# Kernel tuning notes

Hardware: AMD Instinct MI355X
Metric: run time of the kernel (lower is better)

Reference implementation:

```python
import jax, jax.numpy as jnp
import numpy as np

C = 1.0          # Poincare ball curvature
TEMP = 0.1       # softmax temperature
EPS = 1e-15
TANH_CLIP = 1.0 - 1e-5


def setup_inputs() -> dict:
    key = jax.random.key(0)
    ks = jax.random.split(key, 9)
    B, Din, H, D, P = 2048, 1024, 4096, 128, 1000
    inp = {
        "x": jax.random.normal(ks[0], (B, Din), dtype=jnp.float32),
        "W1": jax.random.normal(ks[1], (Din, H), dtype=jnp.float32) / np.sqrt(Din),
        "b1": jnp.zeros((H,), dtype=jnp.float32),
        "W2": jax.random.normal(ks[2], (H, H), dtype=jnp.float32) / np.sqrt(H),
        "b2": jnp.zeros((H,), dtype=jnp.float32),
        "W3": jax.random.normal(ks[3], (H, D), dtype=jnp.float32) / np.sqrt(H),
        "b3": jnp.zeros((D,), dtype=jnp.float32),
        # prototypes: points inside the unit ball (norm ~ 0.2)
        "prototypes": jax.random.normal(ks[4], (P, D), dtype=jnp.float32) * 0.02,
    }
    return inp


def _expmap0(u):
    sqc = np.sqrt(C)
    n = jnp.maximum(jnp.linalg.norm(u, axis=-1, keepdims=True), EPS)
    return jnp.tanh(sqc * n) * u / (sqc * n)


def _logmap0(y):
    sqc = np.sqrt(C)
    n = jnp.maximum(jnp.linalg.norm(y, axis=-1, keepdims=True), EPS)
    arg = jnp.clip(sqc * n, 0.0, TANH_CLIP)
    return jnp.arctanh(arg) * y / (sqc * n)


def _pairwise_dist(proto, xh):
    # dist(x=proto[P,D], y=xh[B,D]) = (2/sqrt(c)) * artanh(sqrt(c)*||(-x) (+) y||)
    # Mobius add norm computed from Gram products only (no [B,P,D] intermediate).
    # a = -proto, b = xh
    a2 = jnp.sum(proto * proto, axis=-1)          # [P]  ||a||^2
    b2 = jnp.sum(xh * xh, axis=-1)                # [B]  ||b||^2
    ab = -jnp.einsum('bd,pd->bp', xh, proto)      # [B,P] <a,b>
    a2_ = a2[None, :]
    b2_ = b2[:, None]
    alpha = 1.0 + 2.0 * C * ab + C * b2_
    beta = 1.0 - C * a2_
    gamma = 1.0 + 2.0 * C * ab + (C * C) * a2_ * b2_
    m2 = (alpha * alpha * a2_ + 2.0 * alpha * beta * ab + beta * beta * b2_) / (gamma * gamma)
    mnorm = jnp.sqrt(jnp.maximum(m2, 0.0))
    sqc = np.sqrt(C)
    arg = jnp.clip(sqc * mnorm, 0.0, TANH_CLIP)
    return (2.0 / sqc) * jnp.arctanh(arg)         # [B,P]


def reference(x, W1, b1, W2, b2, W3, b3, prototypes):
    h = jax.nn.gelu(x @ W1 + b1, approximate=False)
    h = jax.nn.gelu(h @ W2 + b2, approximate=False)
    u = h @ W3 + b3                               # [B,D]
    x_hyp = _expmap0(u)
    dists = _pairwise_dist(prototypes, x_hyp)     # [B,P]
    logits = -dists / TEMP
    pred = jnp.argmax(logits, axis=1)             # [B]
    pred_protos = jax.lax.stop_gradient(prototypes[pred])  # detach, as in torch
    feedback = _logmap0(pred_protos)              # [B,D]
    return logits, feedback
```

## Files before the change

kernel.cpp:

```cpp
#include <hip/hip_runtime.h>
#include <math.h>

#define B_SZ 2048
#define DIN  1024
#define H_SZ 4096
#define D_SZ 128
#define P_SZ 1000
#define PPAD 1024

typedef __attribute__((ext_vector_type(8))) short bf16x8;
typedef __attribute__((ext_vector_type(4))) float f32x4;

__device__ __forceinline__ float gelu_exact(float v) {
    return 0.5f * v * (1.0f + erff(v * 0.70710678118654752f));
}

__device__ __forceinline__ short f2bf(float f) {
    unsigned u = __float_as_uint(f);
    u = (u + 0x7fffu + ((u >> 16) & 1u)) >> 16;
    return (short)u;
}

__device__ __forceinline__ void gload_lds16(const void* g, void* l) {
    __builtin_amdgcn_global_load_lds(
        (__attribute__((address_space(1))) void*)(uintptr_t)g,
        (__attribute__((address_space(3))) void*)(uintptr_t)l,
        16, 0, 0);
}

__global__ __launch_bounds__(256) void cvt_bf16(
    const float* __restrict__ in, short* __restrict__ out, int n)
{
    const int i = (blockIdx.x * 256 + threadIdx.x) * 4;
    if (i + 3 < n) {
        const float4 v = *reinterpret_cast<const float4*>(&in[i]);
        short4 o;
        o.x = f2bf(v.x); o.y = f2bf(v.y); o.z = f2bf(v.z); o.w = f2bf(v.w);
        *reinterpret_cast<short4*>(&out[i]) = o;
    }
}

__global__ __launch_bounds__(256) void transpose_bf16(
    const float* __restrict__ W, short* __restrict__ WT, int K, int N)
{
    __shared__ float t[64][65];
    const int tid = threadIdx.x;
    const int n0 = blockIdx.x * 64, k0 = blockIdx.y * 64;

    #pragma unroll
    for (int i = 0; i < 4; ++i) {
        const int idx = i * 256 + tid;
        const int r  = idx >> 4;
        const int c4 = (idx & 15) * 4;
        const float4 v = *reinterpret_cast<const float4*>(&W[(size_t)(k0 + r) * N + n0 + c4]);
        t[r][c4 + 0] = v.x; t[r][c4 + 1] = v.y; t[r][c4 + 2] = v.z; t[r][c4 + 3] = v.w;
    }
    __syncthreads();

    #pragma unroll
    for (int i = 0; i < 2; ++i) {
        const int idx = i * 256 + tid;
        const int n  = idx >> 3;
        const int kc = (idx & 7) * 8;
        bf16x8 o;
        #pragma unroll
        for (int q = 0; q < 8; ++q) o[q] = f2bf(t[kc + q][n]);
        *reinterpret_cast<bf16x8*>(&WT[(size_t)(n0 + n) * K + k0 + kc]) = o;
    }
}

__global__ __launch_bounds__(128) void proto_prep(
    const float* __restrict__ proto, short* __restrict__ protob,
    float* __restrict__ a2gp)
{
    const int p = blockIdx.x;
    const int d = threadIdx.x;
    const float y = (p < P_SZ) ? proto[(size_t)p * D_SZ + d] : 0.f;
    protob[(size_t)p * D_SZ + d] = f2bf(y);
    float s = y * y;
    #pragma unroll
    for (int off = 32; off; off >>= 1) s += __shfl_down(s, off);
    __shared__ float part[2];
    if ((d & 63) == 0) part[d >> 6] = s;
    __syncthreads();
    if (d == 0) a2gp[p] = part[0] + part[1];
}

template<int EPI>
__global__ __launch_bounds__(512) void gemm_big(
    const short* __restrict__ A, const short* __restrict__ BT,
    const float* __restrict__ bias, void* __restrict__ Cout,
    int M, int N, int K)
{
    extern __shared__ __align__(16) char smem[];

    const int tid  = threadIdx.x;
    const int lane = tid & 63;
    const int wid  = tid >> 6;
    const int row0 = blockIdx.y * 256;
    const int col0 = blockIdx.x * 128;
    const int wm = (wid >> 1) * 64;
    const int wn = (wid & 1) * 64;
    const int lr = lane & 15, kq = lane >> 4;

    const int kpb    = K / gridDim.z;
    const int kstart = blockIdx.z * kpb;
    const int NT = kpb >> 6;

    f32x4 acc[4][4];
    #pragma unroll
    for (int i = 0; i < 4; ++i)
        #pragma unroll
        for (int j = 0; j < 4; ++j) acc[i][j] = (f32x4){0.f, 0.f, 0.f, 0.f};

    const int srow = lane >> 3;
    const int kch  = (lane & 7) ^ srow;
    const short* Ag = A  + (size_t)(row0 + wid * 32 + srow) * K + kstart + kch * 8;
    const short* Bg = BT + (size_t)(col0 + wid * 16 + srow) * K + kstart + kch * 8;

    auto stage = [&](int t) {
        const int buf = t % 3;
        char* sA = smem + buf * 49152;
        char* sB = sA + 32768;
        const int k0 = t << 6;
        #pragma unroll
        for (int ii = 0; ii < 4; ++ii)
            gload_lds16(Ag + (size_t)ii * 8 * K + k0, sA + (wid * 4 + ii) * 1024);
        #pragma unroll
        for (int ii = 0; ii < 2; ++ii)
            gload_lds16(Bg + (size_t)ii * 8 * K + k0, sB + (wid * 2 + ii) * 1024);
    };

    stage(0);
    stage(1);
    asm volatile("s_waitcnt vmcnt(6)" ::: "memory");
    __builtin_amdgcn_s_barrier();
    asm volatile("" ::: "memory");

    for (int t = 0; t < NT; ++t) {
        const bool more = (t + 2) < NT;
        if (more) stage(t + 2);

        const char* sA = smem + (t % 3) * 49152;
        const char* sB = sA + 32768;

        #pragma unroll
        for (int ks = 0; ks < 2; ++ks) {
            bf16x8 af[4], bfv[4];
            #pragma unroll
            for (int i = 0; i < 4; ++i) {
                const int row = wm + i * 16 + lr;
                af[i] = *reinterpret_cast<const bf16x8*>(
                    sA + row * 128 + (((ks * 4 + kq) ^ (lr & 7)) * 16));
            }
            #pragma unroll
            for (int j = 0; j < 4; ++j) {
                const int row = wn + j * 16 + lr;
                bfv[j] = *reinterpret_cast<const bf16x8*>(
                    sB + row * 128 + (((ks * 4 + kq) ^ (lr & 7)) * 16));
            }
            __builtin_amdgcn_s_setprio(1);
            #pragma unroll
            for (int i = 0; i < 4; ++i)
                #pragma unroll
                for (int j = 0; j < 4; ++j)
                    acc[i][j] = __builtin_amdgcn_mfma_f32_16x16x32_bf16(
                        af[i], bfv[j], acc[i][j], 0, 0, 0);
            __builtin_amdgcn_s_setprio(0);
        }

        asm volatile("" ::: "memory");
        if (more) asm volatile("s_waitcnt vmcnt(6) lgkmcnt(0)" ::: "memory");
        else      asm volatile("s_waitcnt vmcnt(0) lgkmcnt(0)" ::: "memory");
        __builtin_amdgcn_s_barrier();
        asm volatile("" ::: "memory");
    }

    #pragma unroll
    for (int j = 0; j < 4; ++j) {
        const int col = col0 + wn + j * 16 + lr;
        const float bv = (EPI == 0) ? bias[col] : 0.f;
        #pragma unroll
        for (int i = 0; i < 4; ++i) {
            #pragma unroll
            for (int q = 0; q < 4; ++q) {
                const int row = row0 + wm + i * 16 + kq * 4 + q;
                if (EPI == 0) {
                    float v = gelu_exact(acc[i][j][q] + bv);
                    ((short*)Cout)[(size_t)row * N + col] = f2bf(v);
                } else {
                    ((float*)Cout)[((size_t)blockIdx.z * M + row) * N + col] = acc[i][j][q];
                }
            }
        }
    }
}

__global__ __launch_bounds__(128) void expmap_kernel(
    const float* __restrict__ up, const float* __restrict__ b3,
    short* __restrict__ xhb, float* __restrict__ rowb2)
{
    const int b = blockIdx.x;
    const int d = threadIdx.x;
    float u = b3[d];
    #pragma unroll
    for (int z = 0; z < 16; ++z)
        u += up[((size_t)z * B_SZ + b) * D_SZ + d];

    float s = u * u;
    #pragma unroll
    for (int off = 32; off; off >>= 1) s += __shfl_down(s, off);
    __shared__ float part[2];
    if ((d & 63) == 0) part[d >> 6] = s;
    __syncthreads();
    const float n2 = part[0] + part[1];

    const float n = fmaxf(sqrtf(n2), 1e-15f);
    const float t = tanhf(n);
    xhb[(size_t)b * D_SZ + d] = f2bf(u * (t / n));
    if (d == 0) rowb2[b] = t * t;
}

__global__ __launch_bounds__(256) void dist_mfma(
    const short* __restrict__ xhb, const short* __restrict__ protob,
    const float* __restrict__ rowb2, const float* __restrict__ a2gp,
    float* __restrict__ logits)
{
    __shared__ __align__(16) char xs[128 * 256];
    __shared__ __align__(16) char ps[64 * 256];

    const int tid  = threadIdx.x;
    const int lane = tid & 63, wid = tid >> 6;
    const int pt = blockIdx.x * 64;
    const int bt = blockIdx.y * 128;
    const int wm = (wid >> 1) * 64;
    const int wn = (wid & 1) * 32;
    const int lr = lane & 15, kq = lane >> 4;

    const int rl = lane >> 4, c = lane & 15;
    #pragma unroll
    for (int i = 0; i < 8; ++i) {
        const int row = wid * 32 + i * 4 + rl;
        const int lc  = (c & 8) | ((c & 7) ^ (row & 7));
        gload_lds16(xhb + (size_t)(bt + row) * D_SZ + lc * 8,
                    xs + (wid * 8 + i) * 1024);
    }
    #pragma unroll
    for (int i = 0; i < 4; ++i) {
        const int row = wid * 16 + i * 4 + rl;
        const int lc  = (c & 8) | ((c & 7) ^ (row & 7));
        gload_lds16(protob + (size_t)(pt + row) * D_SZ + lc * 8,
                    ps + (wid * 4 + i) * 1024);
    }
    __syncthreads();

    f32x4 acc[4][2];
    #pragma unroll
    for (int i = 0; i < 4; ++i)
        #pragma unroll
        for (int j = 0; j < 2; ++j) acc[i][j] = (f32x4){0.f, 0.f, 0.f, 0.f};

    #pragma unroll
    for (int ks = 0; ks < 4; ++ks) {
        const int kslot = ks * 4 + kq;
        bf16x8 af[4], bfv[2];
        #pragma unroll
        for (int i = 0; i < 4; ++i) {
            const int row = wm + i * 16 + lr;
            const int ph = (kslot & 8) | ((kslot & 7) ^ (row & 7));
            af[i] = *reinterpret_cast<const bf16x8*>(xs + row * 256 + ph * 16);
        }
        #pragma unroll
        for (int j = 0; j < 2; ++j) {
            const int row = wn + j * 16 + lr;
            const int ph = (kslot & 8) | ((kslot & 7) ^ (row & 7));
            bfv[j] = *reinterpret_cast<const bf16x8*>(ps + row * 256 + ph * 16);
        }
        #pragma unroll
        for (int i = 0; i < 4; ++i)
            #pragma unroll
            for (int j = 0; j < 2; ++j)
                acc[i][j] = __builtin_amdgcn_mfma_f32_16x16x32_bf16(
                    af[i], bfv[j], acc[i][j], 0, 0, 0);
    }

    #pragma unroll
    for (int j = 0; j < 2; ++j) {
        const int p = pt + wn + j * 16 + lr;
        if (p < P_SZ) {
            const float a2 = a2gp[p];
            #pragma unroll
            for (int i = 0; i < 4; ++i) {
                #pragma unroll
                for (int q = 0; q < 4; ++q) {
                    const int b = bt + wm + i * 16 + kq * 4 + q;
                    const float b2 = rowb2[b];
                    const float ab = -acc[i][j][q];
                    const float alpha = 1.f + 2.f * ab + b2;
                    const float beta  = 1.f - a2;
                    const float gamma = 1.f + 2.f * ab + a2 * b2;
                    const float num = alpha * alpha * a2 + 2.f * alpha * beta * ab + beta * beta * b2;
                    const float m2 = num / (gamma * gamma);
                    const float mn = sqrtf(fmaxf(m2, 0.f));
                    const float arg = fminf(mn, 0.99999f);
                    const float dist = logf((1.f + arg) / (1.f - arg));
                    logits[(size_t)b * P_SZ + p] = -10.f * dist;
                }
            }
        }
    }
}

__global__ __launch_bounds__(256) void head_kernel(
    const float* __restrict__ logits, const float* __restrict__ proto,
    float* __restrict__ fb)
{
    const int b = blockIdx.x;
    const int tid = threadIdx.x;

    float best = -INFINITY; int bi = 0;
    for (int p = tid; p < P_SZ; p += 256) {
        const float v = logits[(size_t)b * P_SZ + p];
        if (v > best) { best = v; bi = p; }
    }
    __shared__ float bv[256];
    __shared__ int   bidx[256];
    bv[tid] = best; bidx[tid] = bi;
    __syncthreads();
    for (int s = 128; s; s >>= 1) {
        if (tid < s) {
            const float ov = bv[tid + s]; const int oi = bidx[tid + s];
            if (ov > bv[tid] || (ov == bv[tid] && oi < bidx[tid])) { bv[tid] = ov; bidx[tid] = oi; }
        }
        __syncthreads();
    }
    const int pred = bidx[0];
    __syncthreads();

    float y = 0.f;
    if (tid < 128) y = proto[(size_t)pred * D_SZ + tid];
    bv[tid] = y * y;
    __syncthreads();
    for (int s = 128; s; s >>= 1) {
        if (tid < s) bv[tid] += bv[tid + s];
        __syncthreads();
    }
    const float n2 = bv[0];
    if (tid < 128) {
        const float n = fmaxf(sqrtf(n2), 1e-15f);
        const float arg = fminf(n, 0.99999f);
        const float at = 0.5f * logf((1.f + arg) / (1.f - arg));
        fb[(size_t)b * D_SZ + tid] = at * (y / n);
    }
}

extern "C" void kernel_launch(void* const* d_in, const int* in_sizes, int n_in,
                              void* d_out, int out_size, void* d_ws, size_t ws_size,
                              hipStream_t stream)
{
    const float* x     = (const float*)d_in[0];
    const float* W1    = (const float*)d_in[1];
    const float* b1    = (const float*)d_in[2];
    const float* W2    = (const float*)d_in[3];
    const float* b2v   = (const float*)d_in[4];
    const float* W3    = (const float*)d_in[5];
    const float* b3    = (const float*)d_in[6];
    const float* proto = (const float*)d_in[7];

    float* logits = (float*)d_out;
    float* fb     = logits + (size_t)B_SZ * P_SZ;

    short* xb     = (short*)d_ws;
    short* w1t    = xb    + (size_t)B_SZ * DIN;
    short* w2t    = w1t   + (size_t)H_SZ * DIN;
    short* w3t    = w2t   + (size_t)H_SZ * H_SZ;
    short* h1     = w3t   + (size_t)D_SZ * H_SZ;
    short* h2     = h1    + (size_t)B_SZ * H_SZ;
    short* xhb    = h2    + (size_t)B_SZ * H_SZ;
    short* protob = xhb   + (size_t)B_SZ * D_SZ;
    float* rowb2  = (float*)(protob + (size_t)PPAD * D_SZ);
    float* a2gp   = rowb2 + B_SZ;
    float* up     = (float*)h1;

    static_cast<void>(hipFuncSetAttribute(
        reinterpret_cast<const void*>(&gemm_big<0>),
        hipFuncAttributeMaxDynamicSharedMemorySize, 3 * 49152));
    static_cast<void>(hipFuncSetAttribute(
        reinterpret_cast<const void*>(&gemm_big<1>),
        hipFuncAttributeMaxDynamicSharedMemorySize, 3 * 49152));

    cvt_bf16<<<(B_SZ * DIN) / 1024, 256, 0, stream>>>(x, xb, B_SZ * DIN);
    transpose_bf16<<<dim3(H_SZ / 64, DIN / 64), 256, 0, stream>>>(W1, w1t, DIN, H_SZ);
    transpose_bf16<<<dim3(H_SZ / 64, H_SZ / 64), 256, 0, stream>>>(W2, w2t, H_SZ, H_SZ);
    transpose_bf16<<<dim3(D_SZ / 64, H_SZ / 64), 256, 0, stream>>>(W3, w3t, H_SZ, D_SZ);
    proto_prep<<<PPAD, 128, 0, stream>>>(proto, protob, a2gp);

    gemm_big<0><<<dim3(H_SZ / 128, B_SZ / 256), 512, 3 * 49152, stream>>>(
        xb, w1t, b1, h1, B_SZ, H_SZ, DIN);
    gemm_big<0><<<dim3(H_SZ / 128, B_SZ / 256), 512, 3 * 49152, stream>>>(
        h1, w2t, b2v, h2, B_SZ, H_SZ, H_SZ);
    gemm_big<1><<<dim3(1, B_SZ / 256, 16), 512, 3 * 49152, stream>>>(
        h2, w3t, nullptr, up, B_SZ, D_SZ, H_SZ);

    expmap_kernel<<<B_SZ, 128, 0, stream>>>(up, b3, xhb, rowb2);
    dist_mfma<<<dim3(PPAD / 64, B_SZ / 128), 256, 0, stream>>>(
        xhb, protob, rowb2, a2gp, logits);
    head_kernel<<<B_SZ, 256, 0, stream>>>(logits, proto, fb);
}
```

Before: 272.0 us.

## Merge prep kernels into one launch and split GEMM k-step with interleaved barriers

Five preprocessing launches (x conversion, three weight transposes, prototype prep) are folded into one kernel that picks its role from the block index. This removes launch gaps and lets the small jobs run alongside the W2 transpose. Separately, the GEMM main loop now reads the first k-half's fragments before issuing the next global-to-LDS stage. It adds block barriers between the two MFMA halves, so LDS reads, global loads and MFMA can interleave across waves, at the cost of more barriers per iteration.

New measurement: 278.6 us. 2.4% more time.

```diff
diff --git a/kernel.cpp b/kernel.cpp
--- a/kernel.cpp
+++ b/kernel.cpp
@@ -28,25 +28,11 @@
         16, 0, 0);
 }
 
-__global__ __launch_bounds__(256) void cvt_bf16(
-    const float* __restrict__ in, short* __restrict__ out, int n)
-{
-    const int i = (blockIdx.x * 256 + threadIdx.x) * 4;
-    if (i + 3 < n) {
-        const float4 v = *reinterpret_cast<const float4*>(&in[i]);
-        short4 o;
-        o.x = f2bf(v.x); o.y = f2bf(v.y); o.z = f2bf(v.z); o.w = f2bf(v.w);
-        *reinterpret_cast<short4*>(&out[i]) = o;
-    }
-}
-
-__global__ __launch_bounds__(256) void transpose_bf16(
-    const float* __restrict__ W, short* __restrict__ WT, int K, int N)
-{
-    __shared__ float t[64][65];
-    const int tid = threadIdx.x;
-    const int n0 = blockIdx.x * 64, k0 = blockIdx.y * 64;
-
+__device__ __forceinline__ void trans_tile(
+    const float* __restrict__ W, short* __restrict__ WT, int K, int N,
+    int bx, int by, int tid, float (*t)[65])
+{
+    const int n0 = bx * 64, k0 = by * 64;
     #pragma unroll
     for (int i = 0; i < 4; ++i) {
         const int idx = i * 256 + tid;
@@ -56,7 +42,6 @@
         t[r][c4 + 0] = v.x; t[r][c4 + 1] = v.y; t[r][c4 + 2] = v.z; t[r][c4 + 3] = v.w;
     }
     __syncthreads();
-
     #pragma unroll
     for (int i = 0; i < 2; ++i) {
         const int idx = i * 256 + tid;
@@ -69,21 +54,47 @@
     }
 }
 
-__global__ __launch_bounds__(128) void proto_prep(
+__global__ __launch_bounds__(256) void prep_kernel(
+    const float* __restrict__ x,     short* __restrict__ xb,
+    const float* __restrict__ W1,    short* __restrict__ w1t,
+    const float* __restrict__ W2,    short* __restrict__ w2t,
+    const float* __restrict__ W3,    short* __restrict__ w3t,
     const float* __restrict__ proto, short* __restrict__ protob,
     float* __restrict__ a2gp)
 {
-    const int p = blockIdx.x;
-    const int d = threadIdx.x;
-    const float y = (p < P_SZ) ? proto[(size_t)p * D_SZ + d] : 0.f;
-    protob[(size_t)p * D_SZ + d] = f2bf(y);
-    float s = y * y;
-    #pragma unroll
-    for (int off = 32; off; off >>= 1) s += __shfl_down(s, off);
-    __shared__ float part[2];
-    if ((d & 63) == 0) part[d >> 6] = s;
-    __syncthreads();
-    if (d == 0) a2gp[p] = part[0] + part[1];
+    __shared__ float t[64][65];
+    __shared__ float part[4];
+    const int b = blockIdx.x;
+    const int tid = threadIdx.x;
+
+    if (b < 2048) {
+        const int i = b * 1024 + tid * 4;
+        const float4 v = *reinterpret_cast<const float4*>(&x[i]);
+        short4 o;
+        o.x = f2bf(v.x); o.y = f2bf(v.y); o.z = f2bf(v.z); o.w = f2bf(v.w);
+        *reinterpret_cast<short4*>(&xb[i]) = o;
+    } else if (b < 3072) {
+        const int tt = b - 2048;
+        trans_tile(W1, w1t, DIN, H_SZ, tt & 63, tt >> 6, tid, t);
+    } else if (b < 7168) {
+        const int tt = b - 3072;
+        trans_tile(W2, w2t, H_SZ, H_SZ, tt & 63, tt >> 6, tid, t);
+    } else if (b < 7296) {
+        const int tt = b - 7168;
+        trans_tile(W3, w3t, H_SZ, D_SZ, tt & 1, tt >> 1, tid, t);
+    } else {
+        const int h = tid >> 7;
+        const int d = tid & 127;
+        const int p = (b - 7296) * 2 + h;
+        const float y = (p < P_SZ) ? proto[(size_t)p * D_SZ + d] : 0.f;
+        protob[(size_t)p * D_SZ + d] = f2bf(y);
+        float s = y * y;
+        #pragma unroll
+        for (int off = 32; off; off >>= 1) s += __shfl_down(s, off);
+        if ((tid & 63) == 0) part[tid >> 6] = s;
+        __syncthreads();
+        if (d == 0) a2gp[p] = part[h * 2] + part[h * 2 + 1];
+    }
 }
 
 template<int EPI>
@@ -131,6 +142,18 @@
             gload_lds16(Bg + (size_t)ii * 8 * K + k0, sB + (wid * 2 + ii) * 1024);
     };
 
+    auto read_frags = [&](const char* sA, const char* sB, int ks,
+                          bf16x8* af, bf16x8* bfv) {
+        #pragma unroll
+        for (int i = 0; i < 4; ++i)
+            af[i] = *reinterpret_cast<const bf16x8*>(
+                sA + (wm + i * 16 + lr) * 128 + (((ks * 4 + kq) ^ (lr & 7)) * 16));
+        #pragma unroll
+        for (int j = 0; j < 4; ++j)
+            bfv[j] = *reinterpret_cast<const bf16x8*>(
+                sB + (wn + j * 16 + lr) * 128 + (((ks * 4 + kq) ^ (lr & 7)) * 16));
+    };
+
     stage(0);
     stage(1);
     asm volatile("s_waitcnt vmcnt(6)" ::: "memory");
@@ -139,41 +162,43 @@
 
     for (int t = 0; t < NT; ++t) {
         const bool more = (t + 2) < NT;
-        if (more) stage(t + 2);
-
         const char* sA = smem + (t % 3) * 49152;
         const char* sB = sA + 32768;
-
-        #pragma unroll
-        for (int ks = 0; ks < 2; ++ks) {
-            bf16x8 af[4], bfv[4];
+        bf16x8 af[4], bfv[4];
+
+        read_frags(sA, sB, 0, af, bfv);
+        if (more) stage(t + 2);
+        asm volatile("" ::: "memory");
+        __builtin_amdgcn_s_barrier();
+        asm volatile("s_waitcnt lgkmcnt(0)" ::: "memory");
+        __builtin_amdgcn_sched_barrier(0);
+        __builtin_amdgcn_s_setprio(1);
+        #pragma unroll
+        for (int i = 0; i < 4; ++i)
             #pragma unroll
-            for (int i = 0; i < 4; ++i) {
-                const int row = wm + i * 16 + lr;
-                af[i] = *reinterpret_cast<const bf16x8*>(
-                    sA + row * 128 + (((ks * 4 + kq) ^ (lr & 7)) * 16));
-            }
+            for (int j = 0; j < 4; ++j)
+                acc[i][j] = __builtin_amdgcn_mfma_f32_16x16x32_bf16(
+                    af[i], bfv[j], acc[i][j], 0, 0, 0);
+        __builtin_amdgcn_s_setprio(0);
+        asm volatile("" ::: "memory");
+        __builtin_amdgcn_s_barrier();
+
+        read_frags(sA, sB, 1, af, bfv);
+        if (more) asm volatile("s_waitcnt vmcnt(6)" ::: "memory");
+        else      asm volatile("s_waitcnt vmcnt(0)" ::: "memory");
+        __builtin_amdgcn_s_barrier();
+        asm volatile("s_waitcnt lgkmcnt(0)" ::: "memory");
+        __builtin_amdgcn_sched_barrier(0);
+        __builtin_amdgcn_s_setprio(1);
+        #pragma unroll
+        for (int i = 0; i < 4; ++i)
             #pragma unroll
-            for (int j = 0; j < 4; ++j) {
-                const int row = wn + j * 16 + lr;
-                bfv[j] = *reinterpret_cast<const bf16x8*>(
-                    sB + row * 128 + (((ks * 4 + kq) ^ (lr & 7)) * 16));
-            }
-            __builtin_amdgcn_s_setprio(1);
-            #pragma unroll
-            for (int i = 0; i < 4; ++i)
-                #pragma unroll
-                for (int j = 0; j < 4; ++j)
-                    acc[i][j] = __builtin_amdgcn_mfma_f32_16x16x32_bf16(
-                        af[i], bfv[j], acc[i][j], 0, 0, 0);
-            __builtin_amdgcn_s_setprio(0);
-        }
-
+            for (int j = 0; j < 4; ++j)
+                acc[i][j] = __builtin_amdgcn_mfma_f32_16x16x32_bf16(
+                    af[i], bfv[j], acc[i][j], 0, 0, 0);
+        __builtin_amdgcn_s_setprio(0);
         asm volatile("" ::: "memory");
-        if (more) asm volatile("s_waitcnt vmcnt(6) lgkmcnt(0)" ::: "memory");
-        else      asm volatile("s_waitcnt vmcnt(0) lgkmcnt(0)" ::: "memory");
         __builtin_amdgcn_s_barrier();
-        asm volatile("" ::: "memory");
     }
 
     #pragma unroll
@@ -389,11 +414,8 @@
         reinterpret_cast<const void*>(&gemm_big<1>),
         hipFuncAttributeMaxDynamicSharedMemorySize, 3 * 49152));
 
-    cvt_bf16<<<(B_SZ * DIN) / 1024, 256, 0, stream>>>(x, xb, B_SZ * DIN);
-    transpose_bf16<<<dim3(H_SZ / 64, DIN / 64), 256, 0, stream>>>(W1, w1t, DIN, H_SZ);
-    transpose_bf16<<<dim3(H_SZ / 64, H_SZ / 64), 256, 0, stream>>>(W2, w2t, H_SZ, H_SZ);
-    transpose_bf16<<<dim3(D_SZ / 64, H_SZ / 64), 256, 0, stream>>>(W3, w3t, H_SZ, D_SZ);
-    proto_prep<<<PPAD, 128, 0, stream>>>(proto, protob, a2gp);
+    prep_kernel<<<7808, 256, 0, stream>>>(x, xb, W1, w1t, W2, w2t, W3, w3t,
+                                          proto, protob, a2gp);
 
     gemm_big<0><<<dim3(H_SZ / 128, B_SZ / 256), 512, 3 * 49152, stream>>>(
         xb, w1t, b1, h1, B_SZ, H_SZ, DIN);
```
